# Performance work log

Measured on AMD Instinct MI355X. Metric: run time of the kernel, lower is better.

## Reference

```python
import jax, jax.numpy as jnp
import numpy as np

NUM_HEAD = 8


def setup_inputs() -> dict:
    key = jax.random.key(0)
    ks = jax.random.split(key, 4)
    B, nd, nh, nw, N, C = 1, 4, 4, 4, 512, 512
    x = jax.random.normal(ks[0], (B, nd, nh, nw, N, C), dtype=jnp.float32)
    w_qkv = jax.random.normal(ks[1], (C, 3 * C), dtype=jnp.float32) / np.sqrt(C).astype(np.float32)
    b_qkv = jnp.zeros((3 * C,), dtype=jnp.float32)
    w_proj = jax.random.normal(ks[2], (C, C), dtype=jnp.float32) / np.sqrt(C).astype(np.float32)
    b_proj = jnp.zeros((C,), dtype=jnp.float32)
    return {"x": x, "w_qkv": w_qkv, "b_qkv": b_qkv, "w_proj": w_proj, "b_proj": b_proj}


def reference(x, w_qkv, b_qkv, w_proj, b_proj):
    B, nd, nh, nw, N, C = x.shape
    hd = C // NUM_HEAD
    # QKV projection, split into q/k/v with per-head layout [B,nd,nh,nw,N,H,hd]
    qkv = (x @ w_qkv + b_qkv).reshape(B, nd, nh, nw, N, 3, NUM_HEAD, hd)
    q = qkv[..., 0, :, :]
    k = qkv[..., 1, :, :]
    v = qkv[..., 2, :, :]
    # Block-local attention. NOTE: original module defines self.scale but never
    # applies it in forward, so no 1/sqrt(hd) scaling here (faithful to source).
    attn = jnp.einsum('...qhd,...khd->...hqk', q, k)  # [B,nd,nh,nw,H,N,N]
    attn = jax.nn.softmax(attn, axis=-1)
    out = jnp.einsum('...hqk,...khd->...qhd', attn, v)  # [B,nd,nh,nw,N,H,hd]
    out = out.reshape(B, nd, nh, nw, N, C)
    return out @ w_proj + b_proj
```

## Files before the change

kernel.cpp:

```cpp
#include <hip/hip_runtime.h>
#include <hip/hip_bf16.h>

typedef _Float16 half8_t __attribute__((ext_vector_type(8)));
typedef _Float16 half4_t __attribute__((ext_vector_type(4)));
typedef _Float16 half2_t __attribute__((ext_vector_type(2)));
typedef float    f32x4   __attribute__((ext_vector_type(4)));
typedef float    f32x16  __attribute__((ext_vector_type(16)));

#define CDIM 512
#define NHEAD 8
#define HD 64
#define NTOK 512
#define NWIN 64
#define TC 1536

__device__ __forceinline__ float fexp2(float x) {
  float r;
  asm("v_exp_f32 %0, %1" : "=v"(r) : "v"(x));
  return r;
}

#define GLL16(g, l)                                                        \
  __builtin_amdgcn_global_load_lds((const __attribute__((address_space(1))) void*)(g), \
                                   (__attribute__((address_space(3))) void*)(l), 16, 0, 0)


__global__ __launch_bounds__(256) void cvt_x(const float* __restrict__ x,
                                             _Float16* __restrict__ x16, int n8) {
  int i = blockIdx.x * 256 + threadIdx.x;
  if (i < n8) {
    float4 v0 = *(const float4*)(x + (size_t)i * 8);
    float4 v1 = *(const float4*)(x + (size_t)i * 8 + 4);
    half8_t h = {(_Float16)v0.x, (_Float16)v0.y, (_Float16)v0.z, (_Float16)v0.w,
                 (_Float16)v1.x, (_Float16)v1.y, (_Float16)v1.z, (_Float16)v1.w};
    *(half8_t*)(x16 + (size_t)i * 8) = h;
  }
}

__global__ __launch_bounds__(256) void prep_weights(
    const float* __restrict__ wqkv, const float* __restrict__ wproj,
    _Float16* __restrict__ wqkvT, _Float16* __restrict__ wprojT) {
  __shared__ _Float16 T[64 * 65];
  int b = blockIdx.x;
  const float* src; _Float16* dst; int Cc, r0, c0; bool blocked;
  if (b < 192) {
    src = wqkv; dst = wqkvT; Cc = 1536; blocked = false;
    c0 = (b % 24) * 64; r0 = (b / 24) * 64;
  } else {
    b -= 192; src = wproj; dst = wprojT; Cc = 512; blocked = true;
    c0 = (b & 7) * 64; r0 = (b >> 3) * 64;
  }
  const int t = threadIdx.x;
#pragma unroll
  for (int i = 0; i < 16; ++i) {
    int idx = i * 256 + t, rr = idx >> 6, cc = idx & 63;
    T[rr * 65 + cc] = (_Float16)src[(size_t)(r0 + rr) * Cc + c0 + cc];
  }
  __syncthreads();
#pragma unroll
  for (int i = 0; i < 2; ++i) {
    int idx = i * 256 + t, ol = idx >> 3, c8 = idx & 7;
    half8_t vv;
#pragma unroll
    for (int e = 0; e < 8; ++e) vv[e] = T[(c8 * 8 + e) * 65 + ol];
    int o = c0 + ol, k = r0 + c8 * 8;
    if (blocked)
      *(half8_t*)(dst + (size_t)(o >> 4) * 8192 + (size_t)(k >> 5) * 512 +
                  (o & 15) * 32 + (k & 24)) = vv;
    else
      *(half8_t*)(dst + (size_t)o * 512 + k) = vv;
  }
}

__global__ __launch_bounds__(512, 2) void gemm1_qkv(
    const _Float16* __restrict__ x16,
    const _Float16* __restrict__ wT,
    const float* __restrict__ bias,
    _Float16* __restrict__ qkv) {
  __shared__ __align__(16) char ring[4 * 32768];
  char* ringB = ring;
  const int tid = threadIdx.x;
  const int l = tid & 63;
  const int wid = tid >> 6;
  const int wr = wid >> 2, wc = wid & 3;
  const int lr = l & 15, g = l >> 4;
  const int koff = ((g ^ ((lr >> 1) & 3)) << 4);
  const int m0 = blockIdx.x * 256;
  const int cb = blockIdx.y * 256;
  const int j = cb >> 9;

  const int srow4 = l >> 2;
  const int schk = (l & 3) ^ ((srow4 >> 1) & 3);
  const size_t aSrc = (size_t)(m0 + wid * 32 + srow4) * 1024 + ((size_t)schk << 4);
  const size_t bSrc = (size_t)(cb + wid * 32 + srow4) * 1024 + ((size_t)schk << 4);

#define ISSUE_G1(KS)                                                              \
  {                                                                               \
    char* sa = ringB + ((KS)&3) * 32768;                                          \
    char* sb = sa + 16384;                                                        \
    _Pragma("unroll") for (int i = 0; i < 2; ++i) {                               \
      GLL16((const char*)x16 + aSrc + (size_t)i * 16384 + (size_t)(KS)*64,        \
            sa + wid * 2048 + i * 1024);                                          \
      GLL16((const char*)wT + bSrc + (size_t)i * 16384 + (size_t)(KS)*64,         \
            sb + wid * 2048 + i * 1024);                                          \
    }                                                                             \
  }

  ISSUE_G1(0) ISSUE_G1(1) ISSUE_G1(2)

  f32x4 acc[8][4] = {};

#define GITER(KS, NW)                                                             \
  {                                                                               \
    asm volatile("s_waitcnt vmcnt(" NW ")" ::: "memory");                         \
    __builtin_amdgcn_sched_barrier(0);                                            \
    asm volatile("s_barrier" ::: "memory");                                       \
    if ((KS) + 3 < 16) ISSUE_G1((KS) + 3)                                         \
    char* sa = ringB + ((KS)&3) * 32768;                                          \
    char* sb = sa + 16384;                                                        \
    half8_t a[8], b[4];                                                           \
    _Pragma("unroll") for (int mt = 0; mt < 8; ++mt)                              \
        a[mt] = *(const half8_t*)(sa + (wr * 128 + mt * 16 + lr) * 64 + koff);    \
    _Pragma("unroll") for (int nt = 0; nt < 4; ++nt)                              \
        b[nt] = *(const half8_t*)(sb + (wc * 64 + nt * 16 + lr) * 64 + koff);     \
    __builtin_amdgcn_s_setprio(1);                                                \
    _Pragma("unroll") for (int mt = 0; mt < 8; ++mt)                              \
        _Pragma("unroll") for (int nt = 0; nt < 4; ++nt)                          \
            acc[mt][nt] =                                                         \
                __builtin_amdgcn_mfma_f32_16x16x32_f16(a[mt], b[nt], acc[mt][nt], 0, 0, 0); \
    __builtin_amdgcn_s_setprio(0);                                                \
  }

  GITER(0, "8")  GITER(1, "8")  GITER(2, "8")  GITER(3, "8")
  GITER(4, "8")  GITER(5, "8")  GITER(6, "8")  GITER(7, "8")
  GITER(8, "8")  GITER(9, "8")  GITER(10, "8") GITER(11, "8")
  GITER(12, "8") GITER(13, "8") GITER(14, "4") GITER(15, "0")

  if (j == 2) {
#pragma unroll
    for (int nt = 0; nt < 4; ++nt) {
      const int ch = cb + wc * 64 + nt * 16 + lr;
      const int h = (ch >> 6) & 7, d = ch & 63;
      const float bvs = bias[ch];
#pragma unroll
      for (int mt = 0; mt < 8; ++mt) {
        const int row = m0 + wr * 128 + mt * 16 + g * 4;
        const int wL = row >> 9, n = row & 511;
        _Float16* panel = qkv + ((size_t)(wL * 24 + 16 + h) << 15);
        const int kg = n >> 4, hh = (n >> 2) & 1, e4 = (n & 8) >> 1;
        half4_t pk = {(_Float16)(acc[mt][nt][0] + bvs), (_Float16)(acc[mt][nt][1] + bvs),
                      (_Float16)(acc[mt][nt][2] + bvs), (_Float16)(acc[mt][nt][3] + bvs)};
        *(half4_t*)(panel + ((size_t)(kg * 2 + hh) * 64 + d) * 8 + e4) = pk;
      }
    }
  } else {
    __syncthreads();
    const float scl = (j == 0) ? 1.44269504f : 1.0f;
    char* CB = ringB;
#pragma unroll
    for (int nt = 0; nt < 4; ++nt) {
      const int chl = wc * 64 + nt * 16 + lr;
      const float bvs = bias[cb + chl];
#pragma unroll
      for (int mt = 0; mt < 8; ++mt) {
#pragma unroll
        for (int r = 0; r < 4; ++r) {
          int nl = wr * 128 + mt * 16 + g * 4 + r;
          *(_Float16*)(CB + nl * 512 + ((chl * 2) ^ ((nl & 7) << 5))) =
              (_Float16)((acc[mt][nt][r] + bvs) * scl);
        }
      }
    }
    __syncthreads();
#pragma unroll
    for (int i = 0; i < 16; ++i) {
      int idx = i * 512 + tid, nl = idx >> 5, c8 = idx & 31;
      half8_t vv = *(const half8_t*)(CB + nl * 512 + ((c8 * 16) ^ ((nl & 7) << 5)));
      int chg = cb + c8 * 8;
      int h = (chg >> 6) & 7, d = chg & 63;
      int ng = m0 + nl, wL = ng >> 9, nn = ng & 511;
      _Float16* panel = qkv + ((size_t)(wL * 24 + j * 8 + h) << 15);
      *(half8_t*)(panel + (size_t)nn * 64 + d) = vv;
    }
  }
}

__global__ __launch_bounds__(512) void attn_win(const _Float16* __restrict__ qkv,
                                                _Float16* __restrict__ obuf) {
  __shared__ __align__(16) char ring[4 * 8192];
  char* ringB = ring;
  const int tid = threadIdx.x;
  const int l = tid & 63;
  const int wid = tid >> 6;
  const int q32 = l & 31;
  const int h2 = l >> 5;
  const int wh = blockIdx.x;
  const int qc = blockIdx.y;
  const int h = wh & 7;
  const int w = wh >> 3;
  const _Float16* Qp = qkv + ((size_t)(w * 24 + h) << 15);
  const _Float16* Kp = qkv + ((size_t)(w * 24 + 8 + h) << 15);
  const _Float16* Vp = qkv + ((size_t)(w * 24 + 16 + h) << 15);
  const int qrow = qc * 256 + wid * 32 + q32;

  const size_t kSrc = (size_t)(l >> 3) * 128 + (size_t)((l & 7) ^ (l >> 3)) * 16;
  const int kof0 = ((0 * 2 + h2) ^ (q32 & 7)) << 4;
  const int kof1 = ((1 * 2 + h2) ^ (q32 & 7)) << 4;
  const int kof2 = ((2 * 2 + h2) ^ (q32 & 7)) << 4;
  const int kof3 = ((3 * 2 + h2) ^ (q32 & 7)) << 4;
  const int voff = 4096 + h2 * 1024 + q32 * 16;

#define ISSUE_SLOT(KT)                                                            \
  {                                                                               \
    char* sb = ringB + ((KT)&3) * 8192;                                           \
    if (wid < 4) {                                                                \
      GLL16((const char*)Kp + (size_t)(KT)*4096 + (size_t)wid * 1024 + kSrc,      \
            sb + wid * 1024);                                                     \
    } else {                                                                      \
      GLL16((const char*)Vp + (size_t)(KT)*4096 + (size_t)(wid - 4) * 1024 + l * 16, \
            sb + 4096 + (wid - 4) * 1024);                                        \
    }                                                                             \
  }

  half8_t qf[4];
#pragma unroll
  for (int j = 0; j < 4; ++j)
    qf[j] = *(const half8_t*)(Qp + (size_t)qrow * 64 + j * 16 + h2 * 8);
  asm volatile("s_waitcnt vmcnt(0)" ::: "memory");

  ISSUE_SLOT(0) ISSUE_SLOT(1) ISSUE_SLOT(2)

  f32x16 o0 = {}, o1 = {};
  float m_run = -1e30f, lsum = 0.f;

#define AITER(KT, NW)                                                             \
  {                                                                               \
    asm volatile("s_waitcnt vmcnt(" NW ")" ::: "memory");                         \
    __builtin_amdgcn_sched_barrier(0);                                            \
    asm volatile("s_barrier" ::: "memory");                                       \
    if ((KT) + 3 < 16) ISSUE_SLOT((KT) + 3)                                       \
    char* sl = ringB + ((KT)&3) * 8192;                                           \
    half8_t kf0 = *(const half8_t*)(sl + q32 * 128 + kof0);                       \
    half8_t kf1 = *(const half8_t*)(sl + q32 * 128 + kof1);                       \
    half8_t kf2 = *(const half8_t*)(sl + q32 * 128 + kof2);                       \
    half8_t kf3 = *(const half8_t*)(sl + q32 * 128 + kof3);                       \
    __builtin_amdgcn_s_setprio(1);                                                \
    f32x16 s = {};                                                                \
    s = __builtin_amdgcn_mfma_f32_32x32x16_f16(kf0, qf[0], s, 0, 0, 0);           \
    s = __builtin_amdgcn_mfma_f32_32x32x16_f16(kf1, qf[1], s, 0, 0, 0);           \
    s = __builtin_amdgcn_mfma_f32_32x32x16_f16(kf2, qf[2], s, 0, 0, 0);           \
    s = __builtin_amdgcn_mfma_f32_32x32x16_f16(kf3, qf[3], s, 0, 0, 0);           \
    __builtin_amdgcn_s_setprio(0);                                                \
    float ma = fmaxf(fmaxf(s[0], s[1]), s[2]);                                    \
    float mb = fmaxf(fmaxf(s[3], s[4]), s[5]);                                    \
    float mc = fmaxf(fmaxf(s[6], s[7]), s[8]);                                    \
    float md = fmaxf(fmaxf(s[9], s[10]), s[11]);                                  \
    float me = fmaxf(fmaxf(s[12], s[13]), s[14]);                                 \
    float mf_ = fmaxf(fmaxf(ma, mb), mc);                                         \
    float mg = fmaxf(fmaxf(md, me), s[15]);                                       \
    float tmax = fmaxf(mf_, mg);                                                  \
    tmax = fmaxf(tmax, __shfl_xor(tmax, 32));                                     \
    if (!__all(tmax <= m_run + 11.5f)) {                                          \
      float mNew = fmaxf(m_run, tmax);                                            \
      float sc = fexp2(m_run - mNew);                                             \
      lsum *= sc;                                                                 \
      _Pragma("unroll") for (int r = 0; r < 16; ++r) { o0[r] *= sc; o1[r] *= sc; }\
      m_run = mNew;                                                               \
    }                                                                             \
    half8_t pf0, pf1;                                                             \
    float tsum = 0.f;                                                             \
    _Pragma("unroll") for (int e = 0; e < 4; ++e) {                               \
      float a0 = fexp2(s[2 * e] - m_run), a1 = fexp2(s[2 * e + 1] - m_run);       \
      tsum += a0 + a1;                                                            \
      ((half2_t*)&pf0)[e] =                                                       \
          __builtin_bit_cast(half2_t, __builtin_amdgcn_cvt_pkrtz(a0, a1));        \
    }                                                                             \
    _Pragma("unroll") for (int e = 0; e < 4; ++e) {                               \
      float a0 = fexp2(s[8 + 2 * e] - m_run), a1 = fexp2(s[9 + 2 * e] - m_run);   \
      tsum += a0 + a1;                                                            \
      ((half2_t*)&pf1)[e] =                                                       \
          __builtin_bit_cast(half2_t, __builtin_amdgcn_cvt_pkrtz(a0, a1));        \
    }                                                                             \
    tsum += __shfl_xor(tsum, 32);                                                 \
    lsum += tsum;                                                                 \
    half8_t vf0 = *(const half8_t*)(sl + voff);                                   \
    half8_t vf1 = *(const half8_t*)(sl + voff + 512);                             \
    half8_t vf2 = *(const half8_t*)(sl + voff + 2048);                            \
    half8_t vf3 = *(const half8_t*)(sl + voff + 2560);                            \
    __builtin_amdgcn_s_setprio(1);                                                \
    o0 = __builtin_amdgcn_mfma_f32_32x32x16_f16(vf0, pf0, o0, 0, 0, 0);           \
    o1 = __builtin_amdgcn_mfma_f32_32x32x16_f16(vf1, pf0, o1, 0, 0, 0);           \
    o0 = __builtin_amdgcn_mfma_f32_32x32x16_f16(vf2, pf1, o0, 0, 0, 0);           \
    o1 = __builtin_amdgcn_mfma_f32_32x32x16_f16(vf3, pf1, o1, 0, 0, 0);           \
    __builtin_amdgcn_s_setprio(0);                                                \
  }

  AITER(0, "2")  AITER(1, "2")  AITER(2, "2")  AITER(3, "2")
  AITER(4, "2")  AITER(5, "2")  AITER(6, "2")  AITER(7, "2")
  AITER(8, "2")  AITER(9, "2")  AITER(10, "2") AITER(11, "2")
  AITER(12, "2") AITER(13, "2") AITER(14, "1") AITER(15, "0")

  const float inv = 1.0f / lsum;
  const size_t rbase = ((size_t)(w * 32 + qc * 16 + wid * 2 + (q32 >> 4))) * 8192 +
                       (size_t)(q32 & 15) * 32 + 4 * h2;
#pragma unroll
  for (int rq = 0; rq < 4; ++rq) {
    half4_t v0, v1;
#pragma unroll
    for (int i = 0; i < 4; ++i) {
      v0[i] = (_Float16)(o0[rq * 4 + i] * inv);
      v1[i] = (_Float16)(o1[rq * 4 + i] * inv);
    }
    *(half4_t*)(obuf + rbase + (size_t)(h * 2 + 0) * 512 + 8 * rq) = v0;
    *(half4_t*)(obuf + rbase + (size_t)(h * 2 + 1) * 512 + 8 * rq) = v1;
  }
}

__global__ __launch_bounds__(256, 3) void gemm2_proj(
    const _Float16* __restrict__ obuf,
    const _Float16* __restrict__ wpT,
    const float* __restrict__ bias,
    float* __restrict__ out) {
  __shared__ __align__(16) char ring[3 * 16384];
  char* ringB = ring;
  const int tid = threadIdx.x;
  const int l = tid & 63;
  const int wid = tid >> 6;
  const int wr = wid >> 1, wc = wid & 1;
  const int lr = l & 15, g = l >> 4;
  const int koff = ((g ^ ((lr >> 1) & 3)) << 4);
  const int m0 = blockIdx.x * 128;
  const int n0 = blockIdx.y * 128;

  const int r4 = l >> 2;
  const int schk = (l & 3) ^ ((r4 >> 1) & 3);
  const size_t laneT = (size_t)r4 * 64 + (size_t)schk * 16;
  const size_t aTile = ((size_t)(blockIdx.x * 8 + wid * 2)) * 16384 + laneT;
  const size_t bTile = ((size_t)(blockIdx.y * 8 + wid * 2)) * 16384 + laneT;

#define ISSUE_G2(KS)                                                              \
  {                                                                               \
    char* sa = ringB + ((KS) % 3) * 16384;                                        \
    char* sbB = sa + 8192;                                                        \
    _Pragma("unroll") for (int i = 0; i < 2; ++i) {                               \
      GLL16((const char*)obuf + aTile + (size_t)i * 16384 + (size_t)(KS)*1024,    \
            sa + wid * 2048 + i * 1024);                                          \
      GLL16((const char*)wpT + bTile + (size_t)i * 16384 + (size_t)(KS)*1024,     \
            sbB + wid * 2048 + i * 1024);                                         \
    }                                                                             \
  }

  ISSUE_G2(0) ISSUE_G2(1)

  f32x4 acc[4][4] = {};

#define G2ITER(KS, NW)                                                            \
  {                                                                               \
    asm volatile("s_waitcnt vmcnt(" NW ")" ::: "memory");                         \
    __builtin_amdgcn_sched_barrier(0);                                            \
    asm volatile("s_barrier" ::: "memory");                                       \
    if ((KS) + 2 < 16) ISSUE_G2((KS) + 2)                                         \
    char* sa = ringB + ((KS) % 3) * 16384;                                        \
    char* sbB = sa + 8192;                                                        \
    half8_t a[4], b[4];                                                           \
    _Pragma("unroll") for (int mt = 0; mt < 4; ++mt)                              \
        a[mt] = *(const half8_t*)(sa + (wr * 64 + mt * 16 + lr) * 64 + koff);     \
    _Pragma("unroll") for (int nt = 0; nt < 4; ++nt)                              \
        b[nt] = *(const half8_t*)(sbB + (wc * 64 + nt * 16 + lr) * 64 + koff);    \
    __builtin_amdgcn_s_setprio(1);                                                \
    _Pragma("unroll") for (int mt = 0; mt < 4; ++mt)                              \
        _Pragma("unroll") for (int nt = 0; nt < 4; ++nt)                          \
            acc[mt][nt] =                                                         \
                __builtin_amdgcn_mfma_f32_16x16x32_f16(a[mt], b[nt], acc[mt][nt], 0, 0, 0); \
    __builtin_amdgcn_s_setprio(0);                                                \
  }

  G2ITER(0, "4")  G2ITER(1, "4")  G2ITER(2, "4")  G2ITER(3, "4")
  G2ITER(4, "4")  G2ITER(5, "4")  G2ITER(6, "4")  G2ITER(7, "4")
  G2ITER(8, "4")  G2ITER(9, "4")  G2ITER(10, "4") G2ITER(11, "4")
  G2ITER(12, "4") G2ITER(13, "4") G2ITER(14, "4") G2ITER(15, "0")

#pragma unroll
  for (int nt = 0; nt < 4; ++nt) {
    int col = n0 + wc * 64 + nt * 16 + lr;
    float bv = bias[col & 511];
#pragma unroll
    for (int mt = 0; mt < 4; ++mt) {
      int row = m0 + wr * 64 + mt * 16 + g * 4;
#pragma unroll
      for (int r = 0; r < 4; ++r)
        out[(size_t)(row + r) * 512 + col] = acc[mt][nt][r] + bv;
    }
  }
}

extern "C" void kernel_launch(void* const* d_in, const int* in_sizes, int n_in,
                              void* d_out, int out_size, void* d_ws, size_t ws_size,
                              hipStream_t stream) {
  const float* x = (const float*)d_in[0];
  const float* wqkv = (const float*)d_in[1];
  const float* bqkv = (const float*)d_in[2];
  const float* wproj = (const float*)d_in[3];
  const float* bproj = (const float*)d_in[4];
  float* out = (float*)d_out;

  _Float16* wqkvT = (_Float16*)d_ws;
  _Float16* wprojT = wqkvT + (size_t)TC * CDIM;
  _Float16* chunkws = wprojT + (size_t)CDIM * CDIM;
  const size_t fixed = ((size_t)TC * CDIM + (size_t)CDIM * CDIM) * sizeof(_Float16);
  const size_t perwin =
      ((size_t)NTOK * CDIM + (size_t)24 * 32768 + (size_t)NTOK * CDIM) * sizeof(_Float16);
  int nw = 64;
  while (nw > 1 && fixed + (size_t)nw * perwin > ws_size) nw >>= 1;

  prep_weights<<<dim3(256), 256, 0, stream>>>(wqkv, wproj, wqkvT, wprojT);
  for (int wbase = 0; wbase < NWIN; wbase += nw) {
    const float* xc = x + (size_t)wbase * NTOK * CDIM;
    float* oc = out + (size_t)wbase * NTOK * CDIM;
    _Float16* x16 = chunkws;
    _Float16* qkvws = chunkws + (size_t)nw * NTOK * CDIM;
    _Float16* obuf = qkvws + (size_t)nw * 24 * 32768;
    const int n8 = nw * NTOK * CDIM / 8;
    cvt_x<<<dim3((n8 + 255) / 256), 256, 0, stream>>>(xc, x16, n8);
    gemm1_qkv<<<dim3(nw * 2, 6), 512, 0, stream>>>(x16, wqkvT, bqkv, qkvws);
    attn_win<<<dim3(nw * 8, 2), 512, 0, stream>>>(qkvws, obuf);
    gemm2_proj<<<dim3(nw * 4, 4), 256, 0, stream>>>(obuf, wprojT, bproj, oc);
  }
}
```

Before: 185.1 us.

## Use blocked fp16 layouts and smaller 128x128 tiles for the QKV GEMM

The x conversion now writes x16 in a 16-row by 32-column blocked layout, and the QKV weights get the same blocked transpose as the projection weights, so every global-to-LDS load is one contiguous 1 KB chunk. The QKV GEMM moves from 256x256 tiles with 512 threads and a 4-stage ring to 128x128 tiles with 256 threads, a 3-stage ring and launch bounds allowing 3 blocks per CU, giving 4x more blocks. The aim is better load coalescing, more occupancy and a smaller tail. In exchange each tile does less operand reuse per byte loaded and the prefetch depth is shallower.

```diff
diff --git a/kernel.cpp b/kernel.cpp
--- a/kernel.cpp
+++ b/kernel.cpp
@@ -26,14 +26,20 @@
 
 
 __global__ __launch_bounds__(256) void cvt_x(const float* __restrict__ x,
-                                             _Float16* __restrict__ x16, int n8) {
-  int i = blockIdx.x * 256 + threadIdx.x;
-  if (i < n8) {
-    float4 v0 = *(const float4*)(x + (size_t)i * 8);
-    float4 v1 = *(const float4*)(x + (size_t)i * 8 + 4);
-    half8_t h = {(_Float16)v0.x, (_Float16)v0.y, (_Float16)v0.z, (_Float16)v0.w,
-                 (_Float16)v1.x, (_Float16)v1.y, (_Float16)v1.z, (_Float16)v1.w};
-    *(half8_t*)(x16 + (size_t)i * 8) = h;
+                                             _Float16* __restrict__ x16) {
+  const int rb = blockIdx.x;
+  const int l = threadIdx.x & 63, wv = threadIdx.x >> 6;
+  const int r4 = l >> 2, c = l & 3;
+  const float* src = x + (size_t)rb * 16 * 512 + (size_t)r4 * 512;
+  _Float16* dst = x16 + (size_t)rb * 8192;
+#pragma unroll
+  for (int i = 0; i < 4; ++i) {
+    int ks = wv * 4 + i;
+    const float4 v0 = *(const float4*)(src + ks * 32 + c * 8);
+    const float4 v1 = *(const float4*)(src + ks * 32 + c * 8 + 4);
+    half8_t hv = {(_Float16)v0.x, (_Float16)v0.y, (_Float16)v0.z, (_Float16)v0.w,
+                  (_Float16)v1.x, (_Float16)v1.y, (_Float16)v1.z, (_Float16)v1.w};
+    *(half8_t*)(dst + ks * 512 + r4 * 32 + c * 8) = hv;
   }
 }
 
@@ -42,12 +48,12 @@
     _Float16* __restrict__ wqkvT, _Float16* __restrict__ wprojT) {
   __shared__ _Float16 T[64 * 65];
   int b = blockIdx.x;
-  const float* src; _Float16* dst; int Cc, r0, c0; bool blocked;
+  const float* src; _Float16* dst; int Cc, r0, c0;
   if (b < 192) {
-    src = wqkv; dst = wqkvT; Cc = 1536; blocked = false;
+    src = wqkv; dst = wqkvT; Cc = 1536;
     c0 = (b % 24) * 64; r0 = (b / 24) * 64;
   } else {
-    b -= 192; src = wproj; dst = wprojT; Cc = 512; blocked = true;
+    b -= 192; src = wproj; dst = wprojT; Cc = 512;
     c0 = (b & 7) * 64; r0 = (b >> 3) * 64;
   }
   const int t = threadIdx.x;
@@ -64,77 +70,75 @@
 #pragma unroll
     for (int e = 0; e < 8; ++e) vv[e] = T[(c8 * 8 + e) * 65 + ol];
     int o = c0 + ol, k = r0 + c8 * 8;
-    if (blocked)
-      *(half8_t*)(dst + (size_t)(o >> 4) * 8192 + (size_t)(k >> 5) * 512 +
-                  (o & 15) * 32 + (k & 24)) = vv;
-    else
-      *(half8_t*)(dst + (size_t)o * 512 + k) = vv;
-  }
-}
-
-__global__ __launch_bounds__(512, 2) void gemm1_qkv(
+    *(half8_t*)(dst + (size_t)(o >> 4) * 8192 + (size_t)(k >> 5) * 512 +
+                (o & 15) * 32 + (k & 24)) = vv;
+  }
+}
+
+__global__ __launch_bounds__(256, 3) void gemm1_qkv(
     const _Float16* __restrict__ x16,
     const _Float16* __restrict__ wT,
     const float* __restrict__ bias,
     _Float16* __restrict__ qkv) {
-  __shared__ __align__(16) char ring[4 * 32768];
+  __shared__ __align__(16) char ring[3 * 16384];
   char* ringB = ring;
   const int tid = threadIdx.x;
   const int l = tid & 63;
   const int wid = tid >> 6;
-  const int wr = wid >> 2, wc = wid & 3;
+  const int wr = wid >> 1, wc = wid & 1;
   const int lr = l & 15, g = l >> 4;
   const int koff = ((g ^ ((lr >> 1) & 3)) << 4);
-  const int m0 = blockIdx.x * 256;
-  const int cb = blockIdx.y * 256;
+  const int m0 = blockIdx.x * 128;
+  const int cb = blockIdx.y * 128;
   const int j = cb >> 9;
 
-  const int srow4 = l >> 2;
-  const int schk = (l & 3) ^ ((srow4 >> 1) & 3);
-  const size_t aSrc = (size_t)(m0 + wid * 32 + srow4) * 1024 + ((size_t)schk << 4);
-  const size_t bSrc = (size_t)(cb + wid * 32 + srow4) * 1024 + ((size_t)schk << 4);
+  const int r4 = l >> 2;
+  const int schk = (l & 3) ^ ((r4 >> 1) & 3);
+  const size_t laneT = (size_t)r4 * 64 + (size_t)schk * 16;
+  const size_t aTile = ((size_t)(blockIdx.x * 8 + wid * 2)) * 16384 + laneT;
+  const size_t bTile = ((size_t)(blockIdx.y * 8 + wid * 2)) * 16384 + laneT;
 
 #define ISSUE_G1(KS)                                                              \
   {                                                                               \
-    char* sa = ringB + ((KS)&3) * 32768;                                          \
-    char* sb = sa + 16384;                                                        \
+    char* sa = ringB + ((KS) % 3) * 16384;                                        \
+    char* sbB = sa + 8192;                                                        \
     _Pragma("unroll") for (int i = 0; i < 2; ++i) {                               \
-      GLL16((const char*)x16 + aSrc + (size_t)i * 16384 + (size_t)(KS)*64,        \
+      GLL16((const char*)x16 + aTile + (size_t)i * 16384 + (size_t)(KS)*1024,     \
             sa + wid * 2048 + i * 1024);                                          \
-      GLL16((const char*)wT + bSrc + (size_t)i * 16384 + (size_t)(KS)*64,         \
-            sb + wid * 2048 + i * 1024);                                          \
-    }                                                                             \
-  }
-
-  ISSUE_G1(0) ISSUE_G1(1) ISSUE_G1(2)
-
-  f32x4 acc[8][4] = {};
+      GLL16((const char*)wT + bTile + (size_t)i * 16384 + (size_t)(KS)*1024,      \
+            sbB + wid * 2048 + i * 1024);                                         \
+    }                                                                             \
+  }
+
+  ISSUE_G1(0) ISSUE_G1(1)
+
+  f32x4 acc[4][4] = {};
 
 #define GITER(KS, NW)                                                             \
   {                                                                               \
     asm volatile("s_waitcnt vmcnt(" NW ")" ::: "memory");                         \
     __builtin_amdgcn_sched_barrier(0);                                            \
     asm volatile("s_barrier" ::: "memory");                                       \
-    if ((KS) + 3 < 16) ISSUE_G1((KS) + 3)                                         \
-    char* sa = ringB + ((KS)&3) * 32768;                                          \
-    char* sb = sa + 16384;                                                        \
-    half8_t a[8], b[4];                                                           \
-    _Pragma("unroll") for (int mt = 0; mt < 8; ++mt)                              \
-        a[mt] = *(const half8_t*)(sa + (wr * 128 + mt * 16 + lr) * 64 + koff);    \
+    if ((KS) + 2 < 16) ISSUE_G1((KS) + 2)                                         \
+    char* sa = ringB + ((KS) % 3) * 16384;                                        \
+    char* sbB = sa + 8192;                                                        \
+    half8_t a[4], b[4];                                                           \
+    _Pragma("unroll") for (int mt = 0; mt < 4; ++mt)                              \
+        a[mt] = *(const half8_t*)(sa + (wr * 64 + mt * 16 + lr) * 64 + koff);     \
     _Pragma("unroll") for (int nt = 0; nt < 4; ++nt)                              \
-        b[nt] = *(const half8_t*)(sb + (wc * 64 + nt * 16 + lr) * 64 + koff);     \
+        b[nt] = *(const half8_t*)(sbB + (wc * 64 + nt * 16 + lr) * 64 + koff);    \
     __builtin_amdgcn_s_setprio(1);                                                \
-    _Pragma("unroll") for (int mt = 0; mt < 8; ++mt)                              \
+    _Pragma("unroll") for (int mt = 0; mt < 4; ++mt)                              \
         _Pragma("unroll") for (int nt = 0; nt < 4; ++nt)                          \
             acc[mt][nt] =                                                         \
                 __builtin_amdgcn_mfma_f32_16x16x32_f16(a[mt], b[nt], acc[mt][nt], 0, 0, 0); \
     __builtin_amdgcn_s_setprio(0);                                                \
   }
 
-  GITER(0, "8")  GITER(1, "8")  GITER(2, "8")  GITER(3, "8")
-  GITER(4, "8")  GITER(5, "8")  GITER(6, "8")  GITER(7, "8")
-  GITER(8, "8")  GITER(9, "8")  GITER(10, "8") GITER(11, "8")
-  GITER(12, "8") GITER(13, "8") GITER(14, "4") GITER(15, "0")
+  GITER(0, "4")  GITER(1, "4")  GITER(2, "4")  GITER(3, "4")
+  GITER(4, "4")  GITER(5, "4")  GITER(6, "4")  GITER(7, "4")
+  GITER(8, "4")  GITER(9, "4")  GITER(10, "4") GITER(11, "4")
+  GITER(12, "4") GITER(13, "4") GITER(14, "4") GITER(15, "0")
 
   if (j == 2) {
 #pragma unroll
@@ -143,8 +147,8 @@
       const int h = (ch >> 6) & 7, d = ch & 63;
       const float bvs = bias[ch];
 #pragma unroll
-      for (int mt = 0; mt < 8; ++mt) {
-        const int row = m0 + wr * 128 + mt * 16 + g * 4;
+      for (int mt = 0; mt < 4; ++mt) {
+        const int row = m0 + wr * 64 + mt * 16 + g * 4;
         const int wL = row >> 9, n = row & 511;
         _Float16* panel = qkv + ((size_t)(wL * 24 + 16 + h) << 15);
         const int kg = n >> 4, hh = (n >> 2) & 1, e4 = (n & 8) >> 1;
@@ -162,20 +166,20 @@
       const int chl = wc * 64 + nt * 16 + lr;
       const float bvs = bias[cb + chl];
 #pragma unroll
-      for (int mt = 0; mt < 8; ++mt) {
+      for (int mt = 0; mt < 4; ++mt) {
 #pragma unroll
         for (int r = 0; r < 4; ++r) {
-          int nl = wr * 128 + mt * 16 + g * 4 + r;
-          *(_Float16*)(CB + nl * 512 + ((chl * 2) ^ ((nl & 7) << 5))) =
+          int nl = wr * 64 + mt * 16 + g * 4 + r;
+          *(_Float16*)(CB + nl * 256 + ((chl * 2) ^ ((nl & 7) << 5))) =
               (_Float16)((acc[mt][nt][r] + bvs) * scl);
         }
       }
     }
     __syncthreads();
 #pragma unroll
-    for (int i = 0; i < 16; ++i) {
-      int idx = i * 512 + tid, nl = idx >> 5, c8 = idx & 31;
-      half8_t vv = *(const half8_t*)(CB + nl * 512 + ((c8 * 16) ^ ((nl & 7) << 5)));
+    for (int i = 0; i < 8; ++i) {
+      int idx = i * 256 + tid, nl = idx >> 4, c8 = idx & 15;
+      half8_t vv = *(const half8_t*)(CB + nl * 256 + ((c8 * 16) ^ ((nl & 7) << 5)));
       int chg = cb + c8 * 8;
       int h = (chg >> 6) & 7, d = chg & 63;
       int ng = m0 + nl, wL = ng >> 9, nn = ng & 511;
@@ -420,9 +424,8 @@
     _Float16* x16 = chunkws;
     _Float16* qkvws = chunkws + (size_t)nw * NTOK * CDIM;
     _Float16* obuf = qkvws + (size_t)nw * 24 * 32768;
-    const int n8 = nw * NTOK * CDIM / 8;
-    cvt_x<<<dim3((n8 + 255) / 256), 256, 0, stream>>>(xc, x16, n8);
-    gemm1_qkv<<<dim3(nw * 2, 6), 512, 0, stream>>>(x16, wqkvT, bqkv, qkvws);
+    cvt_x<<<dim3(nw * 32), 256, 0, stream>>>(xc, x16);
+    gemm1_qkv<<<dim3(nw * 4, 12), 256, 0, stream>>>(x16, wqkvT, bqkv, qkvws);
     attn_win<<<dim3(nw * 8, 2), 512, 0, stream>>>(qkvws, obuf);
     gemm2_proj<<<dim3(nw * 4, 4), 256, 0, stream>>>(obuf, wprojT, bproj, oc);
   }
```

Result: slower. 190.5 us (+2.9%).
